# Kernel optimization log

Measured on AMD Instinct MI355X. Metric: run time of the kernel, lower is better.

The kernel has to match this reference:

```python
import jax, jax.numpy as jnp
import numpy as np

# model dims
V, D, C, H, NL, E, EH = 32000, 256, 2, 8, 2, 8, 1024
B, S = 16, 512
DH = D // H
N = B * S


def _pos_encoding(length, d):
    pos = jnp.arange(length)[:, None].astype(jnp.float32)
    div = jnp.exp(jnp.arange(0, d, 2).astype(jnp.float32) * (-np.log(10000.0) / d))
    pe = jnp.zeros((length, d), dtype=jnp.float32)
    pe = pe.at[:, 0::2].set(jnp.sin(pos * div))
    pe = pe.at[:, 1::2].set(jnp.cos(pos * div))
    return pe


def _ln(x, g, b, eps=1e-5):
    mu = x.mean(-1, keepdims=True)
    var = ((x - mu) ** 2).mean(-1, keepdims=True)
    return (x - mu) / jnp.sqrt(var + eps) * g + b


def setup_inputs():
    key = jax.random.key(0)
    ks = jax.random.split(key, 12)
    n = lambda k, shape, s=0.02: (jax.random.normal(k, shape) * s).astype(jnp.float32)
    return dict(
        x=jax.random.randint(ks[0], (B, S), 0, V),
        emb=n(ks[1], (V, D), 0.1),
        in_proj_w=n(ks[2], (NL, 3 * D, D)),
        in_proj_b=jnp.zeros((NL, 3 * D), jnp.float32),
        out_proj_w=n(ks[3], (NL, D, D)),
        out_proj_b=jnp.zeros((NL, D), jnp.float32),
        ln1_g=jnp.ones((NL, D), jnp.float32), ln1_b=jnp.zeros((NL, D), jnp.float32),
        ln2_g=jnp.ones((NL, D), jnp.float32), ln2_b=jnp.zeros((NL, D), jnp.float32),
        gate_w=n(ks[4], (NL, E, D)), gate_b=jnp.zeros((NL, E), jnp.float32),
        w1=n(ks[5], (NL, E, EH, D)), b1=jnp.zeros((NL, E, EH), jnp.float32),
        w2=n(ks[6], (NL, E, D, EH)), b2=jnp.zeros((NL, E, D), jnp.float32),
        fc1_w=n(ks[7], (128, D), 0.1), fc1_b=jnp.zeros((128,), jnp.float32),
        fc2_w=n(ks[8], (C, 128), 0.1), fc2_b=jnp.zeros((C,), jnp.float32),
    )


def reference(x, emb, in_proj_w, in_proj_b, out_proj_w, out_proj_b,
              ln1_g, ln1_b, ln2_g, ln2_b, gate_w, gate_b,
              w1, b1, w2, b2, fc1_w, fc1_b, fc2_w, fc2_b):
    h = emb[x] * np.sqrt(float(D))                       # [B,S,D]
    h = h + _pos_encoding(S, D)[None]
    pad = h.sum(-1) == 0                                 # key padding mask [B,S]
    for l in range(NL):
        # --- multi-head self-attention ---
        qkv = h @ in_proj_w[l].T + in_proj_b[l]          # [B,S,3D]
        q, k, v = jnp.split(qkv, 3, axis=-1)
        q = q.reshape(B, S, H, DH).transpose(0, 2, 1, 3)
        k = k.reshape(B, S, H, DH).transpose(0, 2, 1, 3)
        v = v.reshape(B, S, H, DH).transpose(0, 2, 1, 3)
        sc = jnp.einsum('bhqd,bhkd->bhqk', q, k) / np.sqrt(float(DH))
        sc = jnp.where(pad[:, None, None, :], -1e9, sc)
        a = jax.nn.softmax(sc, axis=-1)
        ctx = jnp.einsum('bhqk,bhkd->bhqd', a, v).transpose(0, 2, 1, 3).reshape(B, S, D)
        attn_out = ctx @ out_proj_w[l].T + out_proj_b[l]
        h = _ln(h + attn_out, ln1_g[l], ln1_b[l])
        # --- top-1 MoE ---
        xf = h.reshape(N, D)
        gwt = jax.nn.softmax(xf @ gate_w[l].T + gate_b[l], axis=-1)  # [N,E]
        top_idx = jnp.argmax(gwt, axis=-1)                # [N]
        top_w = jnp.max(gwt, axis=-1)                     # [N]
        eh = jax.nn.relu(jnp.einsum('nd,ehd->enh', xf, w1[l]) + b1[l][:, None, :])
        ey = jnp.einsum('enh,edh->end', eh, w2[l]) + b2[l][:, None, :]  # [E,N,D]
        sel = ey[top_idx, jnp.arange(N)]                  # gather routed expert output [N,D]
        moe = (top_w[:, None] * sel).reshape(B, S, D)
        h = _ln(h + moe, ln2_g[l], ln2_b[l])
    m = (~pad)[..., None].astype(h.dtype)                 # [B,S,1]
    pooled = (h * m).sum(1) / jnp.clip(m.sum(1), 1.0)     # masked mean pool [B,D]
    z = jax.nn.relu(pooled @ fc1_w.T + fc1_b)
    return z @ fc2_w.T + fc2_b                            # [B,C]
```

## Files before the change

kernel.cpp:

```cpp
#include <hip/hip_runtime.h>
#include <math.h>

#define D_MODEL 256
#define NTOK    8192
#define SEQ     512
#define NB      16
#define NH      8
#define DHEAD   32
#define NE      8
#define EHID    1024
#define CSTRIDE 32

typedef __attribute__((ext_vector_type(8))) short short8;
typedef __attribute__((ext_vector_type(4))) float floatx4;
typedef unsigned short ushort_t;

__device__ __forceinline__ ushort_t bf16r(float f) {
    unsigned int u = __float_as_uint(f);
    u += 0x7fffu + ((u >> 16) & 1u);
    return (ushort_t)(u >> 16);
}

#define GLD16(gsrc, ldst) \
    __builtin_amdgcn_global_load_lds( \
        (const __attribute__((address_space(1))) void*)(gsrc), \
        (__attribute__((address_space(3))) void*)(ldst), 16, 0, 0)

__global__ __launch_bounds__(256) void wconv_all(
    const float* __restrict__ in_proj_w, const float* __restrict__ out_proj_w,
    const float* __restrict__ w1, const float* __restrict__ w2,
    ushort_t* __restrict__ wball)
{
    const int g = blockIdx.x * 256 + threadIdx.x;
    const float* src; ushort_t* dst; int lo;
    if (g < 98304)        { src = in_proj_w;  dst = wball;           lo = g; }
    else if (g < 131072)  { src = out_proj_w; dst = wball + 393216;  lo = g - 98304; }
    else if (g < 1179648) { src = w1;         dst = wball + 524288;  lo = g - 131072; }
    else                  { src = w2;         dst = wball + 4718592; lo = g - 1179648; }
    float4 v = *(const float4*)(src + (size_t)lo * 4);
    ushort_t o[4] = { bf16r(v.x), bf16r(v.y), bf16r(v.z), bf16r(v.w) };
    *(uint2*)(dst + (size_t)lo * 4) = *(uint2*)o;
}

__global__ __launch_bounds__(256) void embed_kernel(
    const int* __restrict__ x, const float* __restrict__ emb,
    float* __restrict__ h, ushort_t* __restrict__ hb, int* __restrict__ pad)
{
    __shared__ float wred[4];
    const int n = blockIdx.x;
    const int d = threadIdx.x;
    const int wave = d >> 6;
    const int s = n & (SEQ - 1);
    const int tok = x[n];
    float v = emb[tok * D_MODEL + d] * 16.0f;
    const int j = d >> 1;
    const float c = -9.210340371976184f / 256.0f;
    const float div = expf((float)(2 * j) * c);
    const float ang = (float)s * div;
    v += (d & 1) ? cosf(ang) : sinf(ang);
    h[n * D_MODEL + d] = v;
    hb[n * D_MODEL + d] = bf16r(v);
    float sm = v;
    for (int o = 1; o < 64; o <<= 1) sm += __shfl_xor(sm, o);
    if ((d & 63) == 0) wred[wave] = sm;
    __syncthreads();
    if (d == 0) pad[n] = ((wred[0] + wred[1] + wred[2] + wred[3]) == 0.0f) ? 1 : 0;
}

#define GF_RELU    1
#define GF_OUTBF16 2
#define GF_GATHER  4
#define GF_SCATTER 8

__global__ __launch_bounds__(256) void gemm_gl64(
    const ushort_t* __restrict__ A, const ushort_t* __restrict__ Bw,
    const float* __restrict__ bias, void* __restrict__ Cout,
    int M, int N, int K,
    const int* __restrict__ counts,
    const int* __restrict__ perm, const float* __restrict__ topw,
    int flags)
{
    __shared__ ushort_t As[64 * 64];
    __shared__ ushort_t Bs[64 * 64];
    const int e = blockIdx.z;
    int cnt, off = 0;
    if (counts) {
        cnt = counts[e * CSTRIDE];
        if ((int)blockIdx.y * 64 >= cnt) return;
        for (int i = 0; i < e; i++) off += counts[i * CSTRIDE];
    } else { cnt = M; }
    const ushort_t* Bp = Bw + (size_t)e * N * K;
    const float* bp = bias + (size_t)e * N;
    const int m0 = blockIdx.y * 64, n0 = blockIdx.x * 64;
    const int tid = threadIdx.x;
    const int lane = tid & 63, wave = tid >> 6;
    const int r8 = lane >> 3;
    const int p  = lane & 7;
    const int kswz = ((p ^ r8) << 3);
    const int row0 = wave * 16;
    size_t asrc[2], bsrc[2];
#pragma unroll
    for (int c = 0; c < 2; c++) {
        const int gr = m0 + row0 + c * 8 + r8;
        const int grc = (gr < cnt) ? gr : m0;
        asrc[c] = (flags & GF_GATHER) ? (size_t)perm[off + grc] : (size_t)(off + grc);
        bsrc[c] = (size_t)(n0 + row0 + c * 8 + r8);
    }
    const int quad = lane >> 4, fr = lane & 15;
    const int wm = (wave & 1) * 32, wn = (wave >> 1) * 32;
    floatx4 acc[2][2];
#pragma unroll
    for (int i = 0; i < 2; i++)
#pragma unroll
        for (int jj = 0; jj < 2; jj++) acc[i][jj] = (floatx4){0.f, 0.f, 0.f, 0.f};

    for (int k0 = 0; k0 < K; k0 += 64) {
        __syncthreads();
#pragma unroll
        for (int c = 0; c < 2; c++) {
            GLD16(A + asrc[c] * K + k0 + kswz, &As[(row0 + c * 8) * 64]);
            GLD16(Bp + bsrc[c] * K + k0 + kswz, &Bs[(row0 + c * 8) * 64]);
        }
        __syncthreads();
#pragma unroll
        for (int ks = 0; ks < 2; ks++) {
            const int sw = (((ks * 4 + quad) ^ (fr & 7)) << 3);
            short8 fa0 = *(const short8*)&As[(wm + fr) * 64 + sw];
            short8 fa1 = *(const short8*)&As[(wm + 16 + fr) * 64 + sw];
            short8 fb0 = *(const short8*)&Bs[(wn + fr) * 64 + sw];
            short8 fb1 = *(const short8*)&Bs[(wn + 16 + fr) * 64 + sw];
            acc[0][0] = __builtin_amdgcn_mfma_f32_16x16x32_bf16(fa0, fb0, acc[0][0], 0, 0, 0);
            acc[0][1] = __builtin_amdgcn_mfma_f32_16x16x32_bf16(fa0, fb1, acc[0][1], 0, 0, 0);
            acc[1][0] = __builtin_amdgcn_mfma_f32_16x16x32_bf16(fa1, fb0, acc[1][0], 0, 0, 0);
            acc[1][1] = __builtin_amdgcn_mfma_f32_16x16x32_bf16(fa1, fb1, acc[1][1], 0, 0, 0);
        }
    }
    const int crow0 = quad * 4;
    const int ccol = fr;
#pragma unroll
    for (int m = 0; m < 2; m++) {
#pragma unroll
        for (int n = 0; n < 2; n++) {
            const int gcol = n0 + wn + n * 16 + ccol;
            const float bsv = bp[gcol];
#pragma unroll
            for (int r = 0; r < 4; r++) {
                const int grow = m0 + wm + m * 16 + crow0 + r;
                if (grow >= cnt) continue;
                float v = acc[m][n][r] + bsv;
                if (flags & GF_RELU) v = fmaxf(v, 0.f);
                if (flags & GF_SCATTER) {
                    const int tok = perm[off + grow];
                    ((float*)Cout)[(size_t)tok * N + gcol] = v * topw[tok];
                } else if (flags & GF_OUTBF16) {
                    ((ushort_t*)Cout)[(size_t)(off + grow) * N + gcol] = bf16r(v);
                } else {
                    ((float*)Cout)[(size_t)(off + grow) * N + gcol] = v;
                }
            }
        }
    }
}

__global__ __launch_bounds__(256) void oproj_ln(
    const ushort_t* __restrict__ Actx, const ushort_t* __restrict__ Wb,
    const float* __restrict__ bias, float* __restrict__ h,
    ushort_t* __restrict__ hb,
    const float* __restrict__ g, const float* __restrict__ b,
    const float* __restrict__ gw, const float* __restrict__ gb,
    int* __restrict__ top_idx, float* __restrict__ top_w)
{
    __shared__ ushort_t As[16 * 64];
    __shared__ ushort_t Bs[256 * 64];
    __shared__ float lsum[16][4], lsq[16][4];
    __shared__ float gred[16][NE][4];
    const int m0 = blockIdx.x * 16;
    const int tid = threadIdx.x;
    const int lane = tid & 63, wave = tid >> 6;
    const int r8 = lane >> 3, p = lane & 7;
    const int kswz = ((p ^ r8) << 3);
    const int quad = lane >> 4, fr = lane & 15;
    const int wn = wave * 64;
    floatx4 acc[4];
#pragma unroll
    for (int n = 0; n < 4; n++) acc[n] = (floatx4){0.f, 0.f, 0.f, 0.f};

    for (int k0 = 0; k0 < 256; k0 += 64) {
        __syncthreads();
        if (wave < 2)
            GLD16(Actx + (size_t)(m0 + wave * 8 + r8) * 256 + k0 + kswz,
                  &As[(wave * 8) * 64]);
#pragma unroll
        for (int c = 0; c < 8; c++)
            GLD16(Wb + (size_t)(wn + c * 8 + r8) * 256 + k0 + kswz,
                  &Bs[(wn + c * 8) * 64]);
        __syncthreads();
#pragma unroll
        for (int ks = 0; ks < 2; ks++) {
            const int sw = (((ks * 4 + quad) ^ (fr & 7)) << 3);
            short8 fa = *(const short8*)&As[fr * 64 + sw];
#pragma unroll
            for (int n = 0; n < 4; n++) {
                short8 fb = *(const short8*)&Bs[(wn + n * 16 + fr) * 64 + sw];
                acc[n] = __builtin_amdgcn_mfma_f32_16x16x32_bf16(fa, fb, acc[n], 0, 0, 0);
            }
        }
    }
    const int rbase = quad * 4;
    float val[4][4];
#pragma unroll
    for (int n = 0; n < 4; n++) {
        const int col = wn + n * 16 + fr;
        const float bsv = bias[col];
#pragma unroll
        for (int r = 0; r < 4; r++)
            val[r][n] = acc[n][r] + bsv + h[(size_t)(m0 + rbase + r) * 256 + col];
    }
    float s[4], sq[4];
#pragma unroll
    for (int r = 0; r < 4; r++) {
        s[r]  = val[r][0] + val[r][1] + val[r][2] + val[r][3];
        sq[r] = val[r][0] * val[r][0] + val[r][1] * val[r][1]
              + val[r][2] * val[r][2] + val[r][3] * val[r][3];
    }
#pragma unroll
    for (int ox = 1; ox < 16; ox <<= 1)
#pragma unroll
        for (int r = 0; r < 4; r++) {
            s[r] += __shfl_xor(s[r], ox);
            sq[r] += __shfl_xor(sq[r], ox);
        }
    if (fr == 0)
#pragma unroll
        for (int r = 0; r < 4; r++) { lsum[rbase + r][wave] = s[r]; lsq[rbase + r][wave] = sq[r]; }
    __syncthreads();
    float mu[4], rstd[4];
#pragma unroll
    for (int r = 0; r < 4; r++) {
        const int row = rbase + r;
        const float m = (lsum[row][0] + lsum[row][1] + lsum[row][2] + lsum[row][3]) * (1.f / 256.f);
        float v2 = (lsq[row][0] + lsq[row][1] + lsq[row][2] + lsq[row][3]) * (1.f / 256.f) - m * m;
        mu[r] = m;
        rstd[r] = rsqrtf(fmaxf(v2, 0.f) + 1e-5f);
    }
    float o4[4][4];
#pragma unroll
    for (int n = 0; n < 4; n++) {
        const int col = wn + n * 16 + fr;
        const float gc = g[col], bc = b[col];
#pragma unroll
        for (int r = 0; r < 4; r++) {
            const float o = (val[r][n] - mu[r]) * rstd[r] * gc + bc;
            o4[r][n] = o;
            const size_t idx = (size_t)(m0 + rbase + r) * 256 + col;
            h[idx] = o;
            hb[idx] = bf16r(o);
        }
    }
#pragma unroll
    for (int e = 0; e < NE; e++) {
        float ge[4] = {0.f, 0.f, 0.f, 0.f};
#pragma unroll
        for (int n = 0; n < 4; n++) {
            const float gwv = gw[e * 256 + wn + n * 16 + fr];
#pragma unroll
            for (int r = 0; r < 4; r++) ge[r] += o4[r][n] * gwv;
        }
#pragma unroll
        for (int ox = 1; ox < 16; ox <<= 1)
#pragma unroll
            for (int r = 0; r < 4; r++) ge[r] += __shfl_xor(ge[r], ox);
        if (fr == 0)
#pragma unroll
            for (int r = 0; r < 4; r++) gred[rbase + r][e][wave] = ge[r];
    }
    __syncthreads();
    if (tid < 16) {
        const int row = tid;
        float lg[NE];
        float best = -1e30f; int bi = 0;
#pragma unroll
        for (int e = 0; e < NE; e++) {
            lg[e] = gred[row][e][0] + gred[row][e][1] + gred[row][e][2] + gred[row][e][3] + gb[e];
            if (lg[e] > best) { best = lg[e]; bi = e; }
        }
        float ssum = 0.f;
#pragma unroll
        for (int e = 0; e < NE; e++) ssum += __expf(lg[e] - best);
        top_idx[m0 + row] = bi;
        top_w[m0 + row] = 1.f / ssum;
    }
}

__global__ __launch_bounds__(256) void fc2_ln(
    const ushort_t* __restrict__ ehb, const ushort_t* __restrict__ Wb,
    const float* __restrict__ b2, const int* __restrict__ counts,
    const int* __restrict__ perm, const float* __restrict__ topw,
    float* __restrict__ h, ushort_t* __restrict__ hb,
    const float* __restrict__ g, const float* __restrict__ b)
{
    __shared__ ushort_t As[16 * 64];
    __shared__ ushort_t Bs[256 * 64];
    __shared__ float lsum[16][4], lsq[16][4];
    const int e = blockIdx.y;
    const int cnt = counts[e * CSTRIDE];
    const int m0 = blockIdx.x * 16;
    if (m0 >= cnt) return;
    int off = 0;
    for (int i = 0; i < e; i++) off += counts[i * CSTRIDE];
    const ushort_t* Wp = Wb + (size_t)e * 256 * 1024;
    const float* bp = b2 + e * 256;
    const int tid = threadIdx.x;
    const int lane = tid & 63, wave = tid >> 6;
    const int r8 = lane >> 3, p = lane & 7;
    const int kswz = ((p ^ r8) << 3);
    const int quad = lane >> 4, fr = lane & 15;
    const int wn = wave * 64;
    size_t arow = 0;
    if (wave < 2) {
        const int gr = m0 + wave * 8 + r8;
        arow = (size_t)(off + ((gr < cnt) ? gr : m0));
    }
    floatx4 acc[4];
#pragma unroll
    for (int n = 0; n < 4; n++) acc[n] = (floatx4){0.f, 0.f, 0.f, 0.f};

    for (int k0 = 0; k0 < 1024; k0 += 64) {
        __syncthreads();
        if (wave < 2)
            GLD16(ehb + arow * 1024 + k0 + kswz, &As[(wave * 8) * 64]);
#pragma unroll
        for (int c = 0; c < 8; c++)
            GLD16(Wp + (size_t)(wn + c * 8 + r8) * 1024 + k0 + kswz,
                  &Bs[(wn + c * 8) * 64]);
        __syncthreads();
#pragma unroll
        for (int ks = 0; ks < 2; ks++) {
            const int sw = (((ks * 4 + quad) ^ (fr & 7)) << 3);
            short8 fa = *(const short8*)&As[fr * 64 + sw];
#pragma unroll
            for (int n = 0; n < 4; n++) {
                short8 fb = *(const short8*)&Bs[(wn + n * 16 + fr) * 64 + sw];
                acc[n] = __builtin_amdgcn_mfma_f32_16x16x32_bf16(fa, fb, acc[n], 0, 0, 0);
            }
        }
    }
    const int rbase = quad * 4;
    int tokr[4]; bool vld[4]; float twr[4];
#pragma unroll
    for (int r = 0; r < 4; r++) {
        const int grow = m0 + rbase + r;
        vld[r] = grow < cnt;
        tokr[r] = perm[off + (vld[r] ? grow : 0)];
        twr[r] = topw[tokr[r]];
    }
    float val[4][4];
#pragma unroll
    for (int n = 0; n < 4; n++) {
        const int col = wn + n * 16 + fr;
        const float bsv = bp[col];
#pragma unroll
        for (int r = 0; r < 4; r++)
            val[r][n] = vld[r]
                ? (acc[n][r] + bsv) * twr[r] + h[(size_t)tokr[r] * 256 + col]
                : 0.f;
    }
    float s[4], sq[4];
#pragma unroll
    for (int r = 0; r < 4; r++) {
        s[r]  = val[r][0] + val[r][1] + val[r][2] + val[r][3];
        sq[r] = val[r][0] * val[r][0] + val[r][1] * val[r][1]
              + val[r][2] * val[r][2] + val[r][3] * val[r][3];
    }
#pragma unroll
    for (int ox = 1; ox < 16; ox <<= 1)
#pragma unroll
        for (int r = 0; r < 4; r++) {
            s[r] += __shfl_xor(s[r], ox);
            sq[r] += __shfl_xor(sq[r], ox);
        }
    if (fr == 0)
#pragma unroll
        for (int r = 0; r < 4; r++) { lsum[rbase + r][wave] = s[r]; lsq[rbase + r][wave] = sq[r]; }
    __syncthreads();
#pragma unroll
    for (int r = 0; r < 4; r++) {
        if (!vld[r]) continue;
        const int row = rbase + r;
        const float m = (lsum[row][0] + lsum[row][1] + lsum[row][2] + lsum[row][3]) * (1.f / 256.f);
        float v2 = (lsq[row][0] + lsq[row][1] + lsq[row][2] + lsq[row][3]) * (1.f / 256.f) - m * m;
        const float rstd = rsqrtf(fmaxf(v2, 0.f) + 1e-5f);
#pragma unroll
        for (int n = 0; n < 4; n++) {
            const int col = wn + n * 16 + fr;
            const float o = (val[r][n] - m) * rstd * g[col] + b[col];
            const size_t idx = (size_t)tokr[r] * 256 + col;
            h[idx] = o;
            hb[idx] = bf16r(o);
        }
    }
}

__global__ __launch_bounds__(256) void attn_kernel(
    const ushort_t* __restrict__ qkvb, const int* __restrict__ pad,
    ushort_t* __restrict__ ctxb)
{
    __shared__ ushort_t Kt[64 * 40];
    __shared__ ushort_t Vt[32 * 72];
    __shared__ ushort_t Ps[64 * 72];
    __shared__ float padf[512];
    const int tid = threadIdx.x;
    const int lane = tid & 63;
    const int wave = tid >> 6;
    const int quad = lane >> 4;
    const int l16  = lane & 15;
    const int bid = blockIdx.x;
    const int qt = bid & 7;
    const int hh = (bid >> 3) & 7;
    const int b = bid >> 6;
    const int q0 = wave * 16;

    padf[tid]       = (float)pad[b * SEQ + tid];
    padf[tid + 256] = (float)pad[b * SEQ + 256 + tid];

    short8 qfrag = *(const short8*)(qkvb +
        (size_t)(b * SEQ + qt * 64 + q0 + l16) * 768 + hh * 32 + quad * 8);

    const int skey = tid >> 2;
    const int schunk = (tid & 3) * 8;

    floatx4 o0 = {0.f,0.f,0.f,0.f}, o1 = {0.f,0.f,0.f,0.f};
    float lsumr[4] = {0.f, 0.f, 0.f, 0.f};
    const float scale = 0.17677669529663687f;

    for (int t = 0; t < 8; t++) {
        const int kbase = b * SEQ + t * 64;
        __syncthreads();
        uint4 kv = *(const uint4*)(qkvb + (size_t)(kbase + skey) * 768 + 256 + hh * 32 + schunk);
        *(uint4*)&Kt[skey * 40 + schunk] = kv;
        uint4 vv = *(const uint4*)(qkvb + (size_t)(kbase + skey) * 768 + 512 + hh * 32 + schunk);
        ushort_t vs[8]; *(uint4*)vs = vv;
#pragma unroll
        for (int j = 0; j < 8; j++) {
            const int d = schunk + j;
            Vt[d * 72 + (skey ^ ((d >> 3) << 3))] = vs[j];
        }
        __syncthreads();
        floatx4 sfr[4];
#pragma unroll
        for (int fn = 0; fn < 4; fn++) {
            short8 kf = *(const short8*)&Kt[(fn * 16 + l16) * 40 + quad * 8];
            sfr[fn] = __builtin_amdgcn_mfma_f32_16x16x32_bf16(
                qfrag, kf, (floatx4){0.f,0.f,0.f,0.f}, 0, 0, 0);
        }
#pragma unroll
        for (int fn = 0; fn < 4; fn++) {
            const int keyl = fn * 16 + l16;
            const float pv = padf[t * 64 + keyl];
#pragma unroll
            for (int r = 0; r < 4; r++) {
                float pr = (pv != 0.f) ? 0.f : __expf(sfr[fn][r] * scale);
                ushort_t pb = bf16r(pr);
                lsumr[r] += __uint_as_float(((unsigned)pb) << 16);
                Ps[(q0 + quad * 4 + r) * 72 + keyl] = pb;
            }
        }
#pragma unroll
        for (int kc = 0; kc < 2; kc++) {
            short8 pf = *(const short8*)&Ps[(q0 + l16) * 72 + kc * 32 + quad * 8];
            {
                const int d = l16;
                short8 vf = *(const short8*)&Vt[d * 72 + ((kc * 32 + quad * 8) ^ ((d >> 3) << 3))];
                o0 = __builtin_amdgcn_mfma_f32_16x16x32_bf16(pf, vf, o0, 0, 0, 0);
            }
            {
                const int d = 16 + l16;
                short8 vf = *(const short8*)&Vt[d * 72 + ((kc * 32 + quad * 8) ^ ((d >> 3) << 3))];
                o1 = __builtin_amdgcn_mfma_f32_16x16x32_bf16(pf, vf, o1, 0, 0, 0);
            }
        }
    }
#pragma unroll
    for (int r = 0; r < 4; r++) {
        float v = lsumr[r];
        v += __shfl_xor(v, 1); v += __shfl_xor(v, 2);
        v += __shfl_xor(v, 4); v += __shfl_xor(v, 8);
        lsumr[r] = 1.f / v;
    }
    const int nq = b * SEQ + qt * 64 + q0 + quad * 4;
#pragma unroll
    for (int r = 0; r < 4; r++) {
        ushort_t* outp = ctxb + (size_t)(nq + r) * 256 + hh * 32;
        outp[l16]      = bf16r(o0[r] * lsumr[r]);
        outp[16 + l16] = bf16r(o1[r] * lsumr[r]);
    }
}

__global__ __launch_bounds__(256) void bucket_kernel(
    const int* __restrict__ top_idx, int* __restrict__ pos,
    int* __restrict__ counts)
{
    __shared__ int hist[NE];
    __shared__ int base[NE];
    __shared__ int lpos[256];
    const int n = blockIdx.x * 256 + threadIdx.x;
    if (threadIdx.x < NE) hist[threadIdx.x] = 0;
    __syncthreads();
    const int e = top_idx[n];
    lpos[threadIdx.x] = atomicAdd(&hist[e], 1);
    __syncthreads();
    if (threadIdx.x < NE)
        base[threadIdx.x] = atomicAdd(&counts[threadIdx.x * CSTRIDE], hist[threadIdx.x]);
    __syncthreads();
    pos[n] = base[e] + lpos[threadIdx.x];
}

__global__ __launch_bounds__(256) void scatter_perm(
    const int* __restrict__ top_idx, const int* __restrict__ pos,
    const int* __restrict__ counts, int* __restrict__ perm)
{
    __shared__ int offs_s[NE];
    if (threadIdx.x < NE) {
        int a = 0;
        for (int i = 0; i < (int)threadIdx.x; i++) a += counts[i * CSTRIDE];
        offs_s[threadIdx.x] = a;
    }
    __syncthreads();
    const int n = blockIdx.x * 256 + threadIdx.x;
    if (n < NTOK) perm[offs_s[top_idx[n]] + pos[n]] = n;
}

__global__ __launch_bounds__(256) void pool1(
    const float* __restrict__ h, const int* __restrict__ pad,
    float* __restrict__ pooled, float* __restrict__ cntb)
{
    const int b = blockIdx.x, c = blockIdx.y, d = threadIdx.x;
    float s = 0.0f; int cnt = 0;
    for (int i = 0; i < 32; i++) {
        const int idx = b * SEQ + c * 32 + i;
        if (!pad[idx]) { s += h[(size_t)idx * D_MODEL + d]; cnt++; }
    }
    atomicAdd(&pooled[b * D_MODEL + d], s);
    if (d == 0) atomicAdd(&cntb[b], (float)cnt);
}

__global__ __launch_bounds__(128) void cls_kernel(
    const float* __restrict__ pooled, const float* __restrict__ cntb,
    const float* __restrict__ fc1w, const float* __restrict__ fc1b,
    const float* __restrict__ fc2w, const float* __restrict__ fc2b,
    float* __restrict__ out)
{
    __shared__ float zs[128];
    const int b = blockIdx.x;
    const int j = threadIdx.x;
    const float invc = 1.0f / fmaxf(cntb[b], 1.0f);
    float s = 0.0f;
    for (int d = 0; d < D_MODEL; d++) s += pooled[b * D_MODEL + d] * fc1w[j * D_MODEL + d];
    zs[j] = fmaxf(s * invc + fc1b[j], 0.0f);
    __syncthreads();
    if (j < 2) {
        float o = fc2b[j];
        for (int i = 0; i < 128; i++) o += zs[i] * fc2w[j * 128 + i];
        out[b * 2 + j] = o;
    }
}

extern "C" void kernel_launch(void* const* d_in, const int* in_sizes, int n_in,
                              void* d_out, int out_size, void* d_ws, size_t ws_size,
                              hipStream_t stream)
{
    const int*   x          = (const int*)d_in[0];
    const float* emb        = (const float*)d_in[1];
    const float* in_proj_w  = (const float*)d_in[2];
    const float* in_proj_b  = (const float*)d_in[3];
    const float* out_proj_w = (const float*)d_in[4];
    const float* out_proj_b = (const float*)d_in[5];
    const float* ln1_g      = (const float*)d_in[6];
    const float* ln1_b      = (const float*)d_in[7];
    const float* ln2_g      = (const float*)d_in[8];
    const float* ln2_b      = (const float*)d_in[9];
    const float* gate_w     = (const float*)d_in[10];
    const float* gate_b     = (const float*)d_in[11];
    const float* w1         = (const float*)d_in[12];
    const float* b1         = (const float*)d_in[13];
    const float* w2         = (const float*)d_in[14];
    const float* b2         = (const float*)d_in[15];
    const float* fc1_w      = (const float*)d_in[16];
    const float* fc1_b      = (const float*)d_in[17];
    const float* fc2_w      = (const float*)d_in[18];
    const float* fc2_b      = (const float*)d_in[19];
    float* out = (float*)d_out;

    float* ws = (float*)d_ws;
    float*    h      = ws;
    ushort_t* qkvb   = (ushort_t*)(ws + 4194304);
    ushort_t* ctxb   = (ushort_t*)(ws + 7340032);
    ushort_t* ehb    = (ushort_t*)(ws + 4194304);
    ushort_t* hb     = (ushort_t*)(ws + 8388608);
    float*    top_w  = ws + 9437184;
    float*    pooled = ws + 9445376;
    float*    cntb   = ws + 9449472;
    int*      counts = (int*)(ws + 9449488);
    int* ipart   = (int*)(ws + 9450000);
    int* pad     = ipart;
    int* top_idx = ipart + 8192;
    int* pos     = ipart + 16384;
    int* perm    = ipart + 24576;
    ushort_t* wball = (ushort_t*)(ws + 9482768);

    wconv_all<<<8704, 256, 0, stream>>>(in_proj_w, out_proj_w, w1, w2, wball);
    embed_kernel<<<NTOK, 256, 0, stream>>>(x, emb, h, hb, pad);
    hipMemsetAsync(pooled, 0, (4096 + 16 + 2 * NE * CSTRIDE) * sizeof(float), stream);

    for (int l = 0; l < 2; l++) {
        const ushort_t* inb_l  = wball + (size_t)l * 196608;
        const ushort_t* outb_l = wball + 393216 + (size_t)l * 65536;
        const ushort_t* w1b_l  = wball + 524288 + (size_t)l * 2097152;
        const ushort_t* w2b_l  = wball + 4718592 + (size_t)l * 2097152;
        int* counts_l = counts + l * NE * CSTRIDE;

        gemm_gl64<<<dim3(768 / 64, NTOK / 64, 1), 256, 0, stream>>>(
            hb, inb_l, in_proj_b + l * 768, qkvb, NTOK, 768, 256,
            nullptr, nullptr, nullptr, GF_OUTBF16);
        attn_kernel<<<NB * NH * (SEQ / 64), 256, 0, stream>>>(qkvb, pad, ctxb);
        oproj_ln<<<NTOK / 16, 256, 0, stream>>>(
            ctxb, outb_l, out_proj_b + l * 256, h, hb,
            ln1_g + l * 256, ln1_b + l * 256,
            gate_w + l * NE * 256, gate_b + l * NE, top_idx, top_w);
        bucket_kernel<<<NTOK / 256, 256, 0, stream>>>(top_idx, pos, counts_l);
        scatter_perm<<<NTOK / 256, 256, 0, stream>>>(top_idx, pos, counts_l, perm);
        gemm_gl64<<<dim3(EHID / 64, NTOK / 64, NE), 256, 0, stream>>>(
            hb, w1b_l, b1 + l * NE * EHID, ehb, 0, EHID, 256,
            counts_l, perm, nullptr, GF_GATHER | GF_RELU | GF_OUTBF16);
        fc2_ln<<<dim3(NTOK / 16, NE), 256, 0, stream>>>(
            ehb, w2b_l, b2 + l * NE * 256, counts_l, perm, top_w,
            h, hb, ln2_g + l * 256, ln2_b + l * 256);
    }

    pool1<<<dim3(NB, 16), 256, 0, stream>>>(h, pad, pooled, cntb);
    cls_kernel<<<NB, 128, 0, stream>>>(pooled, cntb, fc1_w, fc1_b, fc2_w, fc2_b, out);
}
```

Before: 397.9 us.

## Enlarge fc2_ln row tile from 16 to 64 tokens per block

The fused expert-FC2 + LayerNorm kernel now computes 64 routed tokens per block instead of 16, with each wave holding a 4x4 grid of MFMA accumulators. Each 256x1024 expert weight tile is loaded once per 64 rows rather than per 16, which cuts weight traffic from global to LDS by about 4x and raises MFMA work per LDS load. The cost is higher register pressure, a larger LDS footprint, fewer blocks, and more padding waste on the last tile of each expert.

```diff
diff --git a/kernel.cpp b/kernel.cpp
--- a/kernel.cpp
+++ b/kernel.cpp
@@ -292,19 +292,19 @@
     }
 }
 
-__global__ __launch_bounds__(256) void fc2_ln(
+__global__ __launch_bounds__(256) void fc2_ln64(
     const ushort_t* __restrict__ ehb, const ushort_t* __restrict__ Wb,
     const float* __restrict__ b2, const int* __restrict__ counts,
     const int* __restrict__ perm, const float* __restrict__ topw,
     float* __restrict__ h, ushort_t* __restrict__ hb,
     const float* __restrict__ g, const float* __restrict__ b)
 {
-    __shared__ ushort_t As[16 * 64];
+    __shared__ ushort_t As[64 * 64];
     __shared__ ushort_t Bs[256 * 64];
-    __shared__ float lsum[16][4], lsq[16][4];
+    __shared__ float lsum[64][4], lsq[64][4];
     const int e = blockIdx.y;
     const int cnt = counts[e * CSTRIDE];
-    const int m0 = blockIdx.x * 16;
+    const int m0 = blockIdx.x * 64;
     if (m0 >= cnt) return;
     int off = 0;
     for (int i = 0; i < e; i++) off += counts[i * CSTRIDE];
@@ -316,19 +316,23 @@
     const int kswz = ((p ^ r8) << 3);
     const int quad = lane >> 4, fr = lane & 15;
     const int wn = wave * 64;
-    size_t arow = 0;
-    if (wave < 2) {
-        const int gr = m0 + wave * 8 + r8;
-        arow = (size_t)(off + ((gr < cnt) ? gr : m0));
-    }
-    floatx4 acc[4];
-#pragma unroll
-    for (int n = 0; n < 4; n++) acc[n] = (floatx4){0.f, 0.f, 0.f, 0.f};
+    size_t asrc[2];
+#pragma unroll
+    for (int c = 0; c < 2; c++) {
+        const int gr = m0 + wave * 16 + c * 8 + r8;
+        asrc[c] = (size_t)(off + ((gr < cnt) ? gr : m0));
+    }
+    floatx4 acc[4][4];
+#pragma unroll
+    for (int m = 0; m < 4; m++)
+#pragma unroll
+        for (int n = 0; n < 4; n++) acc[m][n] = (floatx4){0.f, 0.f, 0.f, 0.f};
 
     for (int k0 = 0; k0 < 1024; k0 += 64) {
         __syncthreads();
-        if (wave < 2)
-            GLD16(ehb + arow * 1024 + k0 + kswz, &As[(wave * 8) * 64]);
+#pragma unroll
+        for (int c = 0; c < 2; c++)
+            GLD16(ehb + asrc[c] * 1024 + k0 + kswz, &As[(wave * 16 + c * 8) * 64]);
 #pragma unroll
         for (int c = 0; c < 8; c++)
             GLD16(Wp + (size_t)(wn + c * 8 + r8) * 1024 + k0 + kswz,
@@ -337,66 +341,66 @@
 #pragma unroll
         for (int ks = 0; ks < 2; ks++) {
             const int sw = (((ks * 4 + quad) ^ (fr & 7)) << 3);
-            short8 fa = *(const short8*)&As[fr * 64 + sw];
-#pragma unroll
-            for (int n = 0; n < 4; n++) {
-                short8 fb = *(const short8*)&Bs[(wn + n * 16 + fr) * 64 + sw];
-                acc[n] = __builtin_amdgcn_mfma_f32_16x16x32_bf16(fa, fb, acc[n], 0, 0, 0);
-            }
-        }
-    }
-    const int rbase = quad * 4;
-    int tokr[4]; bool vld[4]; float twr[4];
-#pragma unroll
-    for (int r = 0; r < 4; r++) {
-        const int grow = m0 + rbase + r;
-        vld[r] = grow < cnt;
-        tokr[r] = perm[off + (vld[r] ? grow : 0)];
-        twr[r] = topw[tokr[r]];
-    }
-    float val[4][4];
+            short8 fa[4], fb[4];
+#pragma unroll
+            for (int m = 0; m < 4; m++) fa[m] = *(const short8*)&As[(m * 16 + fr) * 64 + sw];
+#pragma unroll
+            for (int n = 0; n < 4; n++) fb[n] = *(const short8*)&Bs[(wn + n * 16 + fr) * 64 + sw];
+#pragma unroll
+            for (int m = 0; m < 4; m++)
+#pragma unroll
+                for (int n = 0; n < 4; n++)
+                    acc[m][n] = __builtin_amdgcn_mfma_f32_16x16x32_bf16(fa[m], fb[n], acc[m][n], 0, 0, 0);
+        }
+    }
+    float gc[4], bc[4], b2c[4];
 #pragma unroll
     for (int n = 0; n < 4; n++) {
         const int col = wn + n * 16 + fr;
-        const float bsv = bp[col];
-#pragma unroll
-        for (int r = 0; r < 4; r++)
-            val[r][n] = vld[r]
-                ? (acc[n][r] + bsv) * twr[r] + h[(size_t)tokr[r] * 256 + col]
-                : 0.f;
-    }
-    float s[4], sq[4];
-#pragma unroll
-    for (int r = 0; r < 4; r++) {
-        s[r]  = val[r][0] + val[r][1] + val[r][2] + val[r][3];
-        sq[r] = val[r][0] * val[r][0] + val[r][1] * val[r][1]
-              + val[r][2] * val[r][2] + val[r][3] * val[r][3];
-    }
-#pragma unroll
-    for (int ox = 1; ox < 16; ox <<= 1)
+        gc[n] = g[col]; bc[n] = b[col]; b2c[n] = bp[col];
+    }
+#pragma unroll
+    for (int m = 0; m < 4; m++) {
 #pragma unroll
         for (int r = 0; r < 4; r++) {
-            s[r] += __shfl_xor(s[r], ox);
-            sq[r] += __shfl_xor(sq[r], ox);
-        }
-    if (fr == 0)
-#pragma unroll
-        for (int r = 0; r < 4; r++) { lsum[rbase + r][wave] = s[r]; lsq[rbase + r][wave] = sq[r]; }
-    __syncthreads();
-#pragma unroll
-    for (int r = 0; r < 4; r++) {
-        if (!vld[r]) continue;
-        const int row = rbase + r;
-        const float m = (lsum[row][0] + lsum[row][1] + lsum[row][2] + lsum[row][3]) * (1.f / 256.f);
-        float v2 = (lsq[row][0] + lsq[row][1] + lsq[row][2] + lsq[row][3]) * (1.f / 256.f) - m * m;
-        const float rstd = rsqrtf(fmaxf(v2, 0.f) + 1e-5f);
-#pragma unroll
-        for (int n = 0; n < 4; n++) {
-            const int col = wn + n * 16 + fr;
-            const float o = (val[r][n] - m) * rstd * g[col] + b[col];
-            const size_t idx = (size_t)tokr[r] * 256 + col;
-            h[idx] = o;
-            hb[idx] = bf16r(o);
+            const int row = m * 16 + quad * 4 + r;
+            const bool v = (m0 + row) < cnt;
+            const int tok = perm[off + (v ? (m0 + row) : 0)];
+            const float tw = topw[tok];
+            float s = 0.f, sq = 0.f;
+#pragma unroll
+            for (int n = 0; n < 4; n++) {
+                const int col = wn + n * 16 + fr;
+                float vv = v ? (acc[m][n][r] + b2c[n]) * tw + h[(size_t)tok * 256 + col] : 0.f;
+                acc[m][n][r] = vv;
+                s += vv; sq += vv * vv;
+            }
+            for (int ox = 1; ox < 16; ox <<= 1) {
+                s += __shfl_xor(s, ox);
+                sq += __shfl_xor(sq, ox);
+            }
+            if (fr == 0) { lsum[row][wave] = s; lsq[row][wave] = sq; }
+        }
+    }
+    __syncthreads();
+#pragma unroll
+    for (int m = 0; m < 4; m++) {
+#pragma unroll
+        for (int r = 0; r < 4; r++) {
+            const int row = m * 16 + quad * 4 + r;
+            if (m0 + row >= cnt) continue;
+            const int tok = perm[off + m0 + row];
+            const float mu = (lsum[row][0] + lsum[row][1] + lsum[row][2] + lsum[row][3]) * (1.f / 256.f);
+            float v2 = (lsq[row][0] + lsq[row][1] + lsq[row][2] + lsq[row][3]) * (1.f / 256.f) - mu * mu;
+            const float rstd = rsqrtf(fmaxf(v2, 0.f) + 1e-5f);
+#pragma unroll
+            for (int n = 0; n < 4; n++) {
+                const int col = wn + n * 16 + fr;
+                const float o = (acc[m][n][r] - mu) * rstd * gc[n] + bc[n];
+                const size_t idx = (size_t)tok * 256 + col;
+                h[idx] = o;
+                hb[idx] = bf16r(o);
+            }
         }
     }
 }
@@ -632,7 +636,7 @@
         gemm_gl64<<<dim3(EHID / 64, NTOK / 64, NE), 256, 0, stream>>>(
             hb, w1b_l, b1 + l * NE * EHID, ehb, 0, EHID, 256,
             counts_l, perm, nullptr, GF_GATHER | GF_RELU | GF_OUTBF16);
-        fc2_ln<<<dim3(NTOK / 16, NE), 256, 0, stream>>>(
+        fc2_ln64<<<dim3(NTOK / 64, NE), 256, 0, stream>>>(
             ehb, w2b_l, b2 + l * NE * 256, counts_l, perm, top_w,
             h, hb, ln2_g + l * 256, ln2_b + l * 256);
     }
```

Result: slower. 408.7 us (+2.7%).
